# Performance work log

Measured on AMD Instinct MI355X. Metric: run time of the kernel, lower is better.

The kernel has to match this reference:

```python
import jax, jax.numpy as jnp
import numpy as np

B, T, C = 8, 1024, 1024
NH, HD = 16, 64          # num_heads, head_dim (C = NH*HD)
NL = 8                   # num_layers
TPB = 64                 # tokens_per_block (block_causal)
EPS = 1e-5


def setup_inputs() -> dict:
    key = jax.random.key(0)
    ks = jax.random.split(key, 12)
    s = 0.02
    sequences = jax.random.normal(ks[0], (B, T, C), dtype=jnp.float32)
    # block-causal mask: causal OR same-block (tril | block_diag)
    idx = jnp.arange(T)
    mask = (idx[:, None] >= idx[None, :]) | ((idx[:, None] // TPB) == (idx[None, :] // TPB))
    # stacked per-layer params; torch Linear convention: W has shape [out, in]
    d = {
        "sequences": sequences,
        "mask": mask,
        "Wq": jax.random.normal(ks[1], (NL, C, C)) * s, "bq": jnp.zeros((NL, C)),
        "Wk": jax.random.normal(ks[2], (NL, C, C)) * s, "bk": jnp.zeros((NL, C)),
        "Wv": jax.random.normal(ks[3], (NL, C, C)) * s, "bv": jnp.zeros((NL, C)),
        "Wo": jax.random.normal(ks[4], (NL, C, C)) * s, "bo": jnp.zeros((NL, C)),
        "ln1w": jnp.ones((NL, C)), "ln1b": jnp.zeros((NL, C)),
        "ln2w": jnp.ones((NL, C)), "ln2b": jnp.zeros((NL, C)),
        "W1": jax.random.normal(ks[5], (NL, 4 * C, C)) * s, "b1": jnp.zeros((NL, 4 * C)),
        "W2": jax.random.normal(ks[6], (NL, C, 4 * C)) * s, "b2": jnp.zeros((NL, C)),
        "lnfw": jnp.ones((C,)), "lnfb": jnp.zeros((C,)),
    }
    return d


def _layernorm(x, w, b):
    m = jnp.mean(x, axis=-1, keepdims=True)
    v = jnp.mean(jnp.square(x - m), axis=-1, keepdims=True)
    return (x - m) * jax.lax.rsqrt(v + EPS) * w + b


def _linear(x, W, b):  # x: [..., in], W: [out, in]
    return jnp.einsum('...i,oi->...o', x, W) + b


def _attention(h, mask, Wq, bq, Wk, bk, Wv, bv, Wo, bo):
    # h: [B,T,C]
    q = _linear(h, Wq, bq).reshape(B, T, NH, HD)
    k = _linear(h, Wk, bk).reshape(B, T, NH, HD)
    v = _linear(h, Wv, bv).reshape(B, T, NH, HD)
    att = jnp.einsum('bqhd,bkhd->bhqk', q, k) * (HD ** -0.5)
    att = jnp.where(mask, att, -jnp.inf)
    att = jax.nn.softmax(att, axis=-1)
    y = jnp.einsum('bhqk,bkhd->bqhd', att, v).reshape(B, T, C)
    return _linear(y, Wo, bo)


def reference(sequences, mask, Wq, bq, Wk, bk, Wv, bv, Wo, bo,
              ln1w, ln1b, ln2w, ln2b, W1, b1, W2, b2, lnfw, lnfb):
    x = sequences  # dropout p=0
    for i in range(NL):
        h = _layernorm(x, ln1w[i], ln1b[i])
        x = x + _attention(h, mask, Wq[i], bq[i], Wk[i], bk[i], Wv[i], bv[i], Wo[i], bo[i])
        h = _layernorm(x, ln2w[i], ln2b[i])
        h = _linear(h, W1[i], b1[i])
        h = jax.nn.gelu(h, approximate=False)  # torch nn.GELU default = exact erf
        x = x + _linear(h, W2[i], b2[i])
    return _layernorm(x, lnfw, lnfb)
```

## Files before the change

### kernel.cpp

```cpp
#include <hip/hip_runtime.h>
#include <math.h>

typedef unsigned short ushort_t;
typedef __attribute__((ext_vector_type(4))) float f32x4;
typedef __attribute__((ext_vector_type(8))) short short8;

constexpr int BATCH = 8, T = 1024, C = 1024, NH = 16, HD = 64, NL = 8;
constexpr int MROWS = BATCH * T;
constexpr int CS = 3 * C;

#define WAITVM(n) asm volatile("s_waitcnt vmcnt(" #n ")" ::: "memory")
#define WAITLGKM0 asm volatile("s_waitcnt lgkmcnt(0)" ::: "memory")

__device__ __forceinline__ ushort_t f2bf(float f) {
  unsigned u = __builtin_bit_cast(unsigned, f);
  u += 0x7fffu + ((u >> 16) & 1u);
  return (ushort_t)(u >> 16);
}
__device__ __forceinline__ float bf2f(ushort_t u) {
  unsigned v = (unsigned)u << 16;
  return __builtin_bit_cast(float, v);
}

__device__ __forceinline__ void gload_lds16(const ushort_t* g, ushort_t* l) {
  __builtin_amdgcn_global_load_lds(
      (const __attribute__((address_space(1))) unsigned int*)g,
      (__attribute__((address_space(3))) unsigned int*)l, 16, 0, 0);
}

__global__ __launch_bounds__(256, 8)
void cvt_kernel(const float* __restrict__ in, ushort_t* __restrict__ out)
{
  int g = blockIdx.x * 256 + threadIdx.x;
  f32x4 a = ((const f32x4*)(in + (size_t)g * 8))[0];
  f32x4 b = ((const f32x4*)(in + (size_t)g * 8))[1];
  short8 o;
#pragma unroll
  for (int e = 0; e < 4; ++e) { o[e] = (short)f2bf(a[e]); o[e + 4] = (short)f2bf(b[e]); }
  *(short8*)(out + (size_t)g * 8) = o;
}

__global__ __launch_bounds__(256, 8)
void convw_kernel(const float* __restrict__ Wq, const float* __restrict__ Wk,
                  const float* __restrict__ Wv, const float* __restrict__ Wo,
                  const float* __restrict__ W1, const float* __restrict__ W2,
                  const float* __restrict__ bq, const float* __restrict__ bk,
                  const float* __restrict__ bv,
                  ushort_t* __restrict__ wqkv, ushort_t* __restrict__ wo,
                  ushort_t* __restrict__ w1, ushort_t* __restrict__ w2,
                  float* __restrict__ bqkv)
{
  if (blockIdx.x == 6144) {
    int t = threadIdx.x;
    if (t < 384) {
      const float* s = (t < 128) ? (bq + t * 8)
                     : (t < 256) ? (bk + (t - 128) * 8)
                                 : (bv + (t - 256) * 8);
      f32x4 a = ((const f32x4*)s)[0], b = ((const f32x4*)s)[1];
      ((f32x4*)(bqkv + t * 8))[0] = a;
      ((f32x4*)(bqkv + t * 8))[1] = b;
    }
    return;
  }
  int g = blockIdx.x * 256 + threadIdx.x;
  const float* src;
  ushort_t* dst;
  if (g < 393216) {
    int which = g >> 17;
    int r = g & 131071;
    src = (which == 0 ? Wq : which == 1 ? Wk : Wv) + (size_t)r * 8;
    dst = wqkv + (size_t)g * 8;
  } else if (g < 524288) {
    int r = g - 393216;
    src = Wo + (size_t)r * 8; dst = wo + (size_t)r * 8;
  } else if (g < 1048576) {
    int r = g - 524288;
    src = W1 + (size_t)r * 8; dst = w1 + (size_t)r * 8;
  } else {
    int r = g - 1048576;
    src = W2 + (size_t)r * 8; dst = w2 + (size_t)r * 8;
  }
  f32x4 a = ((const f32x4*)src)[0], b = ((const f32x4*)src)[1];
  short8 o;
#pragma unroll
  for (int e = 0; e < 4; ++e) { o[e] = (short)f2bf(a[e]); o[e + 4] = (short)f2bf(b[e]); }
  *(short8*)dst = o;
}

template<int MODE>
__global__ __launch_bounds__(256, 4)
void gemm97(const ushort_t* __restrict__ A, const ushort_t* __restrict__ Wb,
            const float* __restrict__ bias, ushort_t* __restrict__ outb,
            ushort_t* __restrict__ resid, int K, int N, int nbn)
{
  __shared__ __align__(16) ushort_t Sm[2 * 128 * 64];
  ushort_t* As = Sm;
  ushort_t* Bs = Sm + 128 * 64;

  const int tid = threadIdx.x;
  const int lane = tid & 63, wave = tid >> 6;
  const int wm = wave >> 1, wn = wave & 1;
  const int l15 = lane & 15, l4 = lane >> 4;

  const int xcd = blockIdx.x & 7;
  const int local = blockIdx.x >> 3;
  const int grp = local >> 5, rem = local & 31;
  const int bm = xcd * 8 + (rem >> 2);
  const int bn = grp * 4 + (rem & 3);
  const long bm0 = (long)bm * 128;
  const long bn0 = (long)bn * 128;

  const ushort_t* srcA[4]; const ushort_t* srcB[4]; int dst4[4];
#pragma unroll
  for (int j = 0; j < 4; ++j) {
    int cidx = j * 256 + tid;
    int row = cidx >> 3;
    int cl = (cidx & 7) ^ (row & 7);
    srcA[j] = A + (size_t)(bm0 + row) * K + cl * 8;
    srcB[j] = Wb + (size_t)(bn0 + row) * K + cl * 8;
    dst4[j] = cidx * 8;
  }
  int aoff[2][4], boff[2][4];
#pragma unroll
  for (int ks = 0; ks < 2; ++ks) {
#pragma unroll
    for (int i = 0; i < 4; ++i) {
      int ra = wm * 64 + i * 16 + l15;
      aoff[ks][i] = ra * 64 + (((ks * 4 + l4) ^ (ra & 7)) << 3);
      int rb = wn * 64 + i * 16 + l15;
      boff[ks][i] = rb * 64 + (((ks * 4 + l4) ^ (rb & 7)) << 3);
    }
  }

  f32x4 acc[4][4] = {};
  const int nt = K >> 6;

  for (int t = 0; t < nt; ++t) {
    __syncthreads();
    const int kt = t << 6;
#pragma unroll
    for (int j = 0; j < 4; ++j) {
      gload_lds16(srcA[j] + kt, &As[dst4[j]]);
      gload_lds16(srcB[j] + kt, &Bs[dst4[j]]);
    }
    __syncthreads();
#pragma unroll
    for (int ks = 0; ks < 2; ++ks) {
      short8 af[4], bfr[4];
#pragma unroll
      for (int i = 0; i < 4; ++i) {
        af[i] = *(const short8*)&As[aoff[ks][i]];
        bfr[i] = *(const short8*)&Bs[boff[ks][i]];
      }
#pragma unroll
      for (int mi = 0; mi < 4; ++mi)
#pragma unroll
        for (int ni = 0; ni < 4; ++ni)
          acc[mi][ni] = __builtin_amdgcn_mfma_f32_16x16x32_bf16(
              af[mi], bfr[ni], acc[mi][ni], 0, 0, 0);
    }
  }
  __syncthreads();

  float* fl = (float*)Sm + wave * (16 * 68);
  const long grow0 = bm0 + wm * 64;
  const long gcol0 = bn0 + wn * 64;
  const int c8 = lane & 7;
  const f32x4 bb0 = *(const f32x4*)&bias[gcol0 + c8 * 8];
  const f32x4 bb1 = *(const f32x4*)&bias[gcol0 + c8 * 8 + 4];

#pragma unroll
  for (int mi = 0; mi < 4; ++mi) {
#pragma unroll
    for (int ni = 0; ni < 4; ++ni)
#pragma unroll
      for (int r = 0; r < 4; ++r)
        fl[(l4 * 4 + r) * 68 + ni * 16 + l15] = acc[mi][ni][r];
#pragma unroll
    for (int pass = 0; pass < 2; ++pass) {
      int row = pass * 8 + (lane >> 3);
      f32x4 v0 = *(const f32x4*)&fl[row * 68 + c8 * 8];
      f32x4 v1 = *(const f32x4*)&fl[row * 68 + c8 * 8 + 4];
      v0 += bb0; v1 += bb1;
      const long grow = grow0 + mi * 16 + row;
      if (MODE == 1) {
#pragma unroll
        for (int e = 0; e < 4; ++e) {
          v0[e] = 0.5f * v0[e] * (1.0f + erff(v0[e] * 0.70710678118f));
          v1[e] = 0.5f * v1[e] * (1.0f + erff(v1[e] * 0.70710678118f));
        }
      }
      if (MODE == 2) {
        ushort_t* rp = resid + (size_t)grow * N + gcol0 + c8 * 8;
        short8 rv = *(const short8*)rp;
        short8 o;
#pragma unroll
        for (int e = 0; e < 4; ++e) {
          o[e]     = (short)f2bf(bf2f((ushort_t)rv[e]) + v0[e]);
          o[e + 4] = (short)f2bf(bf2f((ushort_t)rv[e + 4]) + v1[e]);
        }
        *(short8*)rp = o;
      } else {
        short8 o;
#pragma unroll
        for (int e = 0; e < 4; ++e) { o[e] = (short)f2bf(v0[e]); o[e + 4] = (short)f2bf(v1[e]); }
        *(short8*)&outb[(size_t)grow * N + gcol0 + c8 * 8] = o;
      }
    }
  }
}

__global__ __launch_bounds__(256, 4)
void attn_kernel(const ushort_t* __restrict__ qkv, ushort_t* __restrict__ y)
{
  __shared__ __align__(16) ushort_t Ks[2][64 * 64];
  __shared__ __align__(16) ushort_t Vts[2][64 * 64];
  __shared__ __align__(16) ushort_t Ps[64 * 64];
  const int tid = threadIdx.x;
  const int lane = tid & 63, wave = tid >> 6;
  const int l15 = lane & 15, l4 = lane >> 4;
  const int w16 = wave * 16;
  const int bh = blockIdx.x & 127, qpair = blockIdx.x >> 7;
  const int h = bh & 15, b = bh >> 4;
  const int qoff = h * HD, koff = C + h * HD, voff = 2 * C + h * HD;
  const int kvr = tid & 63, dc = tid >> 6;
  const float SC = 0.125f * 1.44269504f;

#pragma unroll
  for (int half = 0; half < 2; ++half) {
    const int qb = half == 0 ? qpair : 15 - qpair;
    const int nkv = qb + 1;
    const size_t qrow0 = (size_t)(b * T + qb * 64);

    short8 aq[2];
#pragma unroll
    for (int ks = 0; ks < 2; ++ks)
      aq[ks] = *(const short8*)(qkv + (qrow0 + w16 + l15) * CS + qoff + ks * 32 + l4 * 8);

    f32x4 o[4] = {};
    float lrun[4] = {0.f, 0.f, 0.f, 0.f};

    {
      const size_t krow0 = (size_t)(b * T);
#pragma unroll
      for (int j = 0; j < 2; ++j) {
        int cidx = j * 256 + tid;
        int row = cidx >> 3, cl = (cidx & 7) ^ (row & 7);
        gload_lds16(qkv + (krow0 + row) * CS + koff + cl * 8, &Ks[0][cidx * 8]);
      }
    }
    short8 vreg0, vreg1;
    vreg0 = *(const short8*)(qkv + ((size_t)(b * T) + kvr) * CS + voff + dc * 8);
    vreg1 = *(const short8*)(qkv + ((size_t)(b * T) + kvr) * CS + voff + (dc + 4) * 8);
    WAITVM(2);
    __builtin_amdgcn_s_barrier();

    for (int t = 0; t < nkv; ++t) {
      const int buf = t & 1;
      const bool more = (t + 1 < nkv);
      short8 vnext0, vnext1;
      if (more) {
        const size_t krow1 = (size_t)(b * T + (t + 1) * 64);
#pragma unroll
        for (int j = 0; j < 2; ++j) {
          int cidx = j * 256 + tid;
          int row = cidx >> 3, cl = (cidx & 7) ^ (row & 7);
          gload_lds16(qkv + (krow1 + row) * CS + koff + cl * 8, &Ks[buf ^ 1][cidx * 8]);
        }
        vnext0 = *(const short8*)(qkv + (krow1 + kvr) * CS + voff + dc * 8);
        vnext1 = *(const short8*)(qkv + (krow1 + kvr) * CS + voff + (dc + 4) * 8);
      }

      f32x4 s[4] = {};
#pragma unroll
      for (int ks = 0; ks < 2; ++ks) {
#pragma unroll
        for (int n = 0; n < 4; ++n) {
          int br = n * 16 + l15;
          int pb = (ks * 4 + l4) ^ (br & 7);
          short8 bk2 = *(const short8*)&Ks[buf][br * 64 + pb * 8];
          s[n] = __builtin_amdgcn_mfma_f32_16x16x32_bf16(aq[ks], bk2, s[n], 0, 0, 0);
        }
      }

#pragma unroll
      for (int i = 0; i < 8; ++i) {
        int d0 = dc * 8 + i;
        Vts[buf][d0 * 64 + (((kvr >> 3) ^ (d0 & 7)) << 3) + (kvr & 7)] = (ushort_t)vreg0[i];
        int d1 = (dc + 4) * 8 + i;
        Vts[buf][d1 * 64 + (((kvr >> 3) ^ (d1 & 7)) << 3) + (kvr & 7)] = (ushort_t)vreg1[i];
      }
      vreg0 = vnext0; vreg1 = vnext1;

#pragma unroll
      for (int r = 0; r < 4; ++r) {
        float rowsum = 0.f;
        int qr = w16 + l4 * 4 + r;
#pragma unroll
        for (int n = 0; n < 4; ++n) {
          float pv = exp2f(s[n][r] * SC);
          rowsum += pv;
          int kv = n * 16 + l15;
          Ps[qr * 64 + (((kv >> 3) ^ (qr & 7)) << 3) + (kv & 7)] = f2bf(pv);
        }
#pragma unroll
        for (int d = 1; d < 16; d <<= 1) rowsum += __shfl_xor(rowsum, d, 16);
        lrun[r] += rowsum;
      }

      WAITLGKM0;
      __builtin_amdgcn_s_barrier();

#pragma unroll
      for (int ks = 0; ks < 2; ++ks) {
        int arow = w16 + l15;
        int pa = (ks * 4 + l4) ^ (arow & 7);
        short8 ap = *(const short8*)&Ps[arow * 64 + pa * 8];
#pragma unroll
        for (int n = 0; n < 4; ++n) {
          int vr = n * 16 + l15;
          int pb = (ks * 4 + l4) ^ (vr & 7);
          short8 bvv = *(const short8*)&Vts[buf][vr * 64 + pb * 8];
          o[n] = __builtin_amdgcn_mfma_f32_16x16x32_bf16(ap, bvv, o[n], 0, 0, 0);
        }
      }

      if (more) { WAITVM(2); }
      __builtin_amdgcn_s_barrier();
    }

#pragma unroll
    for (int n = 0; n < 4; ++n) {
#pragma unroll
      for (int r = 0; r < 4; ++r) {
        float val = o[n][r] / lrun[r];
        y[(qrow0 + w16 + l4 * 4 + r) * C + h * HD + n * 16 + l15] = f2bf(val);
      }
    }
    __builtin_amdgcn_s_barrier();
  }
}

template<int OUTBF16>
__global__ __launch_bounds__(256, 4)
void ln_kernel(const ushort_t* __restrict__ x, const float* __restrict__ w,
               const float* __restrict__ bprm, void* __restrict__ out)
{
  const size_t row = blockIdx.x;
  const int tid = threadIdx.x;
  ushort4 xu = ((const ushort4*)(x + row * 1024))[tid];
  f32x4 xv;
  xv[0] = bf2f(xu.x); xv[1] = bf2f(xu.y); xv[2] = bf2f(xu.z); xv[3] = bf2f(xu.w);
  float s1 = xv[0] + xv[1] + xv[2] + xv[3];
  float s2 = xv[0] * xv[0] + xv[1] * xv[1] + xv[2] * xv[2] + xv[3] * xv[3];
#pragma unroll
  for (int m = 1; m < 64; m <<= 1) {
    s1 += __shfl_xor(s1, m);
    s2 += __shfl_xor(s2, m);
  }
  __shared__ float red[8];
  const int wave = tid >> 6, lane = tid & 63;
  if (lane == 0) { red[wave * 2] = s1; red[wave * 2 + 1] = s2; }
  __syncthreads();
  s1 = red[0] + red[2] + red[4] + red[6];
  s2 = red[1] + red[3] + red[5] + red[7];
  const float mean = s1 * (1.f / 1024.f);
  const float var = s2 * (1.f / 1024.f) - mean * mean;
  const float rstd = rsqrtf(var + 1e-5f);
  f32x4 wv = ((const f32x4*)w)[tid];
  f32x4 bv = ((const f32x4*)bprm)[tid];
  f32x4 ov;
#pragma unroll
  for (int c2 = 0; c2 < 4; ++c2) ov[c2] = (xv[c2] - mean) * rstd * wv[c2] + bv[c2];
  if (OUTBF16) {
    ushort4 u;
    u.x = f2bf(ov[0]); u.y = f2bf(ov[1]); u.z = f2bf(ov[2]); u.w = f2bf(ov[3]);
    ((ushort4*)out)[row * 256 + tid] = u;
  } else {
    ((f32x4*)out)[row * 256 + tid] = ov;
  }
}

extern "C" void kernel_launch(void* const* d_in, const int* in_sizes, int n_in,
                              void* d_out, int out_size, void* d_ws, size_t ws_size,
                              hipStream_t stream)
{
  const float* seq  = (const float*)d_in[0];
  const float* Wq   = (const float*)d_in[2];  const float* bq = (const float*)d_in[3];
  const float* Wk   = (const float*)d_in[4];  const float* bk = (const float*)d_in[5];
  const float* Wv   = (const float*)d_in[6];  const float* bv = (const float*)d_in[7];
  const float* Wo   = (const float*)d_in[8];  const float* bo = (const float*)d_in[9];
  const float* ln1w = (const float*)d_in[10]; const float* ln1b = (const float*)d_in[11];
  const float* ln2w = (const float*)d_in[12]; const float* ln2b = (const float*)d_in[13];
  const float* W1   = (const float*)d_in[14]; const float* b1 = (const float*)d_in[15];
  const float* W2   = (const float*)d_in[16]; const float* b2 = (const float*)d_in[17];
  const float* lnfw = (const float*)d_in[18]; const float* lnfb = (const float*)d_in[19];

  char* ws = (char*)d_ws;
  size_t off = 0;
  ushort_t* X = (ushort_t*)(ws + off); off += (size_t)MROWS * C * 2;
  ushort_t* Hb = (ushort_t*)(ws + off);  off += (size_t)MROWS * C * 2;
  ushort_t* Yb = (ushort_t*)(ws + off);  off += (size_t)MROWS * C * 2;
  ushort_t* BIG = (ushort_t*)(ws + off); off += (size_t)MROWS * 4 * C * 2;
  ushort_t* wqkv = (ushort_t*)(ws + off); off += (size_t)3 * C * C * 2;
  ushort_t* wo   = (ushort_t*)(ws + off); off += (size_t)C * C * 2;
  ushort_t* w1   = (ushort_t*)(ws + off); off += (size_t)4 * C * C * 2;
  ushort_t* w2   = (ushort_t*)(ws + off); off += (size_t)4 * C * C * 2;
  float* bqkv = (float*)(ws + off);       off += (size_t)3 * C * 4;
  ushort_t* QKVb = BIG;
  ushort_t* Gb = BIG;

  const dim3 blk(256);
  const dim3 gCvt(4096);
  const dim3 gQKV(1536);
  const dim3 gWo(512);
  const dim3 gW1(2048);
  const dim3 gW2(512);
  const dim3 gAttn(1024);
  const dim3 gConv(6145);

  cvt_kernel<<<gCvt, blk, 0, stream>>>(seq, X);

  for (int i = 0; i < NL; ++i) {
    const size_t w1Off = (size_t)i * C * C;
    const size_t w4Off = (size_t)i * 4 * C * C;
    convw_kernel<<<gConv, blk, 0, stream>>>(Wq + w1Off, Wk + w1Off, Wv + w1Off,
                                            Wo + w1Off, W1 + w4Off, W2 + w4Off,
                                            bq + i * C, bk + i * C, bv + i * C,
                                            wqkv, wo, w1, w2, bqkv);
    ln_kernel<1><<<MROWS, blk, 0, stream>>>(X, ln1w + i * C, ln1b + i * C, Hb);
    gemm97<0><<<gQKV, blk, 0, stream>>>(Hb, wqkv, bqkv, QKVb, nullptr, C, CS, 24);
    attn_kernel<<<gAttn, blk, 0, stream>>>(QKVb, Yb);
    gemm97<2><<<gWo, blk, 0, stream>>>(Yb, wo, bo + i * C, nullptr, X, C, C, 8);
    ln_kernel<1><<<MROWS, blk, 0, stream>>>(X, ln2w + i * C, ln2b + i * C, Hb);
    gemm97<1><<<gW1, blk, 0, stream>>>(Hb, w1, b1 + (size_t)i * 4 * C, Gb, nullptr, C, 4 * C, 32);
    gemm97<2><<<gW2, blk, 0, stream>>>(Gb, w2, b2 + i * C, nullptr, X, 4 * C, C, 8);
  }
  ln_kernel<0><<<MROWS, blk, 0, stream>>>(X, lnfw, lnfb, (float*)d_out);
}
```

Before: 2.640 ms.

## Prefetch V two tiles ahead, drop mid-loop barrier, defer row-sum reduction

The attention loop now loads V tiles two iterations ahead and writes the transposed V into the next LDS buffer during the current iteration, so that buffer is ready before the end-of-iteration barrier. The barrier between writing P and the PV MFMA is removed, since each wave reads back only the P rows it wrote itself. The cross-lane shuffle reduction of the softmax row sum moves out of the loop and runs once at the end. The aim is fewer barriers, fewer shuffles and better hiding of global-load latency, at the cost of more live registers and extra prologue work.

```diff
diff --git a/kernel.cpp b/kernel.cpp
--- a/kernel.cpp
+++ b/kernel.cpp
@@ -231,6 +231,7 @@
     const int qb = half == 0 ? qpair : 15 - qpair;
     const int nkv = qb + 1;
     const size_t qrow0 = (size_t)(b * T + qb * 64);
+    const size_t krow0 = (size_t)(b * T);
 
     short8 aq[2];
 #pragma unroll
@@ -238,37 +239,52 @@
       aq[ks] = *(const short8*)(qkv + (qrow0 + w16 + l15) * CS + qoff + ks * 32 + l4 * 8);
 
     f32x4 o[4] = {};
-    float lrun[4] = {0.f, 0.f, 0.f, 0.f};
-
-    {
-      const size_t krow0 = (size_t)(b * T);
-#pragma unroll
-      for (int j = 0; j < 2; ++j) {
-        int cidx = j * 256 + tid;
-        int row = cidx >> 3, cl = (cidx & 7) ^ (row & 7);
-        gload_lds16(qkv + (krow0 + row) * CS + koff + cl * 8, &Ks[0][cidx * 8]);
-      }
-    }
-    short8 vreg0, vreg1;
-    vreg0 = *(const short8*)(qkv + ((size_t)(b * T) + kvr) * CS + voff + dc * 8);
-    vreg1 = *(const short8*)(qkv + ((size_t)(b * T) + kvr) * CS + voff + (dc + 4) * 8);
-    WAITVM(2);
+    float lsum[4] = {0.f, 0.f, 0.f, 0.f};
+
+    short8 vc0 = *(const short8*)(qkv + (krow0 + kvr) * CS + voff + dc * 8);
+    short8 vc1 = *(const short8*)(qkv + (krow0 + kvr) * CS + voff + (dc + 4) * 8);
+#pragma unroll
+    for (int j = 0; j < 2; ++j) {
+      int cidx = j * 256 + tid;
+      int row = cidx >> 3, cl = (cidx & 7) ^ (row & 7);
+      gload_lds16(qkv + (krow0 + row) * CS + koff + cl * 8, &Ks[0][cidx * 8]);
+    }
+#pragma unroll
+    for (int i = 0; i < 8; ++i) {
+      int d0 = dc * 8 + i;
+      Vts[0][d0 * 64 + (((kvr >> 3) ^ (d0 & 7)) << 3) + (kvr & 7)] = (ushort_t)vc0[i];
+      int d1 = (dc + 4) * 8 + i;
+      Vts[0][d1 * 64 + (((kvr >> 3) ^ (d1 & 7)) << 3) + (kvr & 7)] = (ushort_t)vc1[i];
+    }
+    if (nkv > 1) {
+      vc0 = *(const short8*)(qkv + (krow0 + 64 + kvr) * CS + voff + dc * 8);
+      vc1 = *(const short8*)(qkv + (krow0 + 64 + kvr) * CS + voff + (dc + 4) * 8);
+      WAITVM(2);
+    } else {
+      WAITVM(0);
+    }
+    WAITLGKM0;
     __builtin_amdgcn_s_barrier();
 
     for (int t = 0; t < nkv; ++t) {
       const int buf = t & 1;
-      const bool more = (t + 1 < nkv);
-      short8 vnext0, vnext1;
+      const bool more  = (t + 1 < nkv);
+      const bool more2 = (t + 2 < nkv);
+
       if (more) {
-        const size_t krow1 = (size_t)(b * T + (t + 1) * 64);
+        const size_t krow1 = krow0 + (size_t)(t + 1) * 64;
 #pragma unroll
         for (int j = 0; j < 2; ++j) {
           int cidx = j * 256 + tid;
           int row = cidx >> 3, cl = (cidx & 7) ^ (row & 7);
           gload_lds16(qkv + (krow1 + row) * CS + koff + cl * 8, &Ks[buf ^ 1][cidx * 8]);
         }
-        vnext0 = *(const short8*)(qkv + (krow1 + kvr) * CS + voff + dc * 8);
-        vnext1 = *(const short8*)(qkv + (krow1 + kvr) * CS + voff + (dc + 4) * 8);
+      }
+      short8 vn0, vn1;
+      if (more2) {
+        const size_t krow2 = krow0 + (size_t)(t + 2) * 64;
+        vn0 = *(const short8*)(qkv + (krow2 + kvr) * CS + voff + dc * 8);
+        vn1 = *(const short8*)(qkv + (krow2 + kvr) * CS + voff + (dc + 4) * 8);
       }
 
       f32x4 s[4] = {};
@@ -283,33 +299,30 @@
         }
       }
 
-#pragma unroll
-      for (int i = 0; i < 8; ++i) {
-        int d0 = dc * 8 + i;
-        Vts[buf][d0 * 64 + (((kvr >> 3) ^ (d0 & 7)) << 3) + (kvr & 7)] = (ushort_t)vreg0[i];
-        int d1 = (dc + 4) * 8 + i;
-        Vts[buf][d1 * 64 + (((kvr >> 3) ^ (d1 & 7)) << 3) + (kvr & 7)] = (ushort_t)vreg1[i];
-      }
-      vreg0 = vnext0; vreg1 = vnext1;
+      if (more) {
+#pragma unroll
+        for (int i = 0; i < 8; ++i) {
+          int d0 = dc * 8 + i;
+          Vts[buf ^ 1][d0 * 64 + (((kvr >> 3) ^ (d0 & 7)) << 3) + (kvr & 7)] = (ushort_t)vc0[i];
+          int d1 = (dc + 4) * 8 + i;
+          Vts[buf ^ 1][d1 * 64 + (((kvr >> 3) ^ (d1 & 7)) << 3) + (kvr & 7)] = (ushort_t)vc1[i];
+        }
+        vc0 = vn0; vc1 = vn1;
+      }
 
 #pragma unroll
       for (int r = 0; r < 4; ++r) {
-        float rowsum = 0.f;
         int qr = w16 + l4 * 4 + r;
 #pragma unroll
         for (int n = 0; n < 4; ++n) {
           float pv = exp2f(s[n][r] * SC);
-          rowsum += pv;
+          lsum[r] += pv;
           int kv = n * 16 + l15;
           Ps[qr * 64 + (((kv >> 3) ^ (qr & 7)) << 3) + (kv & 7)] = f2bf(pv);
         }
-#pragma unroll
-        for (int d = 1; d < 16; d <<= 1) rowsum += __shfl_xor(rowsum, d, 16);
-        lrun[r] += rowsum;
       }
 
       WAITLGKM0;
-      __builtin_amdgcn_s_barrier();
 
 #pragma unroll
       for (int ks = 0; ks < 2; ++ks) {
@@ -325,15 +338,21 @@
         }
       }
 
-      if (more) { WAITVM(2); }
+      if (more2)      { WAITVM(2); }
+      else if (more)  { WAITVM(0); }
       __builtin_amdgcn_s_barrier();
     }
 
 #pragma unroll
+    for (int r = 0; r < 4; ++r)
+#pragma unroll
+      for (int d = 1; d < 16; d <<= 1) lsum[r] += __shfl_xor(lsum[r], d, 16);
+
+#pragma unroll
     for (int n = 0; n < 4; ++n) {
 #pragma unroll
       for (int r = 0; r < 4; ++r) {
-        float val = o[n][r] / lrun[r];
+        float val = o[n][r] / lsum[r];
         y[(qrow0 + w16 + l4 * 4 + r) * C + h * HD + n * 16 + l15] = f2bf(val);
       }
     }
```

New measurement: 2.613 ms. About the same (-1.0%).
